# Kernel tuning notes

Hardware: AMD Instinct MI355X
Metric: run time of the kernel (lower is better)

## Reference

```python
import jax, jax.numpy as jnp
import numpy as np

# ---- cfg constants (JDE / YOLOv4-tracking style) ----
STRIDES = (8.0, 16.0, 32.0)
TRAIN_SIZE = 608.0
LEVELS = 3
NUM_ANCHORS = 4
EMB_DIM = 208
CONF_THRESH = 0.5
NMS_IOU = 0.45
K_LEVEL = 300   # proposals kept per level after confidence filtering
MAX_PROP = 500  # final padded proposal count per image
_ANCHORS = np.array([
    [[8, 24], [11, 34], [16, 48], [23, 68]],
    [[32, 96], [45, 135], [64, 192], [90, 271]],
    [[128, 384], [180, 540], [256, 640], [512, 640]],
], dtype=np.float32)  # [LEVELS, NUM_ANCHORS, 2] in pixels


def _decode_level(pred, emb, anchors_px, stride):
    """pred [B,A,H,W,6], emb [B,H,W,E] -> [B, A*H*W, 4+1+E] (xyxy in [0,1], conf, l2-norm emb)."""
    B, A, H, W, _ = pred.shape
    conf = jax.nn.softmax(pred[..., 4:6], axis=-1)[..., 1:2]  # [B,A,H,W,1]
    anc = anchors_px / stride  # anchors in grid units, [A,2]
    gy, gx = jnp.meshgrid(jnp.arange(H, dtype=pred.dtype),
                          jnp.arange(W, dtype=pred.dtype), indexing="ij")
    aw = anc[:, 0][:, None, None]  # [A,1,1]
    ah = anc[:, 1][:, None, None]
    # JDE-style delta decode: offsets scaled by anchor size, exp size decode
    x = pred[..., 0] * aw + gx
    y = pred[..., 1] * ah + gy
    w = jnp.exp(pred[..., 2]) * aw
    h = jnp.exp(pred[..., 3]) * ah
    scale = stride / TRAIN_SIZE  # back to pixels, then normalize by train size
    x1 = jnp.clip((x - 0.5 * w) * scale, 0.0, 1.0)
    y1 = jnp.clip((y - 0.5 * h) * scale, 0.0, 1.0)
    x2 = jnp.clip((x + 0.5 * w) * scale, 0.0, 1.0)
    y2 = jnp.clip((y + 0.5 * h) * scale, 0.0, 1.0)
    box = jnp.stack([x1, y1, x2, y2], axis=-1)  # [B,A,H,W,4]
    # tile embedding over anchors and l2-normalize (tf.math.l2_normalize, eps on sum of squares)
    pe = jnp.broadcast_to(emb[:, None], (B, A, H, W, emb.shape[-1]))
    n2 = jnp.sum(pe * pe, axis=-1, keepdims=True)
    pe = pe * jax.lax.rsqrt(jnp.maximum(n2, 1e-12))
    preds = jnp.concatenate([box, conf, pe], axis=-1)  # [B,A,H,W,4+1+E]
    return preds.reshape(B, A * H * W, preds.shape[-1])


def _conf_topk(props):
    """Confidence threshold + keep top K_LEVEL per image (zero-padded). props [B,N,D]."""
    s = props[..., 4]
    sm = jnp.where(s > CONF_THRESH, s, 0.0)
    top_s, top_i = jax.lax.top_k(sm, K_LEVEL)
    g = jnp.take_along_axis(props, top_i[..., None], axis=1)  # [B,K,D]
    return g * (top_s > 0.0)[..., None].astype(props.dtype)


def _nms_one(props):
    """Greedy NMS for one image. props [N,D] -> [MAX_PROP,D] zero-padded."""
    sc_in = props[:, 4]
    order = jnp.argsort(-sc_in)
    p = props[order]                      # sorted by score desc
    b, sc = p[:, :4], p[:, 4]
    N = b.shape[0]
    area = (b[:, 2] - b[:, 0]) * (b[:, 3] - b[:, 1])
    ix1 = jnp.maximum(b[:, None, 0], b[None, :, 0])
    iy1 = jnp.maximum(b[:, None, 1], b[None, :, 1])
    ix2 = jnp.minimum(b[:, None, 2], b[None, :, 2])
    iy2 = jnp.minimum(b[:, None, 3], b[None, :, 3])
    inter = jnp.clip(ix2 - ix1, 0.0) * jnp.clip(iy2 - iy1, 0.0)
    iou = inter / (area[:, None] + area[None, :] - inter + 1e-9)  # [N,N]
    idxs = jnp.arange(N)
    keep0 = sc > 0.0
    def step(keep, i):
        row = jnp.take(iou, i, axis=0)
        ki = jnp.take(keep, i)
        sup = ki & (row > NMS_IOU) & (idxs > i)
        return keep & jnp.logical_not(sup), None
    keep, _ = jax.lax.scan(step, keep0, idxs)
    keep = keep & (sc > 0.0)
    rank = jnp.cumsum(keep) - 1
    dest = jnp.where(keep & (rank < MAX_PROP), rank, MAX_PROP)  # out-of-range -> dropped
    out = jnp.zeros((MAX_PROP, p.shape[1]), p.dtype).at[dest].set(p, mode="drop")
    return out


def _forward(pred0, pred1, pred2, emb0, emb1, emb2):
    preds = (pred0, pred1, pred2)
    embs = (emb0, emb1, emb2)
    levels = []
    for i in range(LEVELS):
        pr = _decode_level(preds[i], embs[i], jnp.asarray(_ANCHORS[i]), STRIDES[i])
        levels.append(_conf_topk(pr))
    props = jnp.concatenate(levels, axis=1)        # [B, 3*K_LEVEL, 4+1+E]
    out = jax.vmap(_nms_one)(props)                # [B, MAX_PROP, 4+1+E]
    # entry_stop_gradients: grads only through non-zero (valid) entries
    mask = (jnp.sum(out[..., :4], axis=-1) != 0.0).astype(out.dtype)[..., None]
    return out * mask + jax.lax.stop_gradient(out) * (1.0 - mask)


def setup_inputs() -> dict:
    key = jax.random.key(0)
    ks = jax.random.split(key, 6)
    B = 16
    sizes = [76, 38, 19]  # TRAIN_SIZE // stride
    d = {}
    for i, hw in enumerate(sizes):
        d[f"pred{i}"] = jax.random.normal(ks[i], (B, NUM_ANCHORS, hw, hw, 6), jnp.float32)
        d[f"emb{i}"] = jax.random.normal(ks[3 + i], (B, hw, hw, EMB_DIM), jnp.float32)
    return d


def reference(pred0, pred1, pred2, emb0, emb1, emb2):
    return _forward(pred0, pred1, pred2, emb0, emb1, emb2)
```

## Files before the change

### kernel.cpp

```cpp
#include <hip/hip_runtime.h>

typedef unsigned long long u64;
typedef unsigned int u32;

#define KLVL 300
#define NPROP 900
#define MAXPROP 500
#define DDIM 213
#define EDIM 208

__constant__ float c_anc[3][4][2] = {
  {{1.0f, 3.0f}, {1.375f, 4.25f}, {2.0f, 6.0f}, {2.875f, 8.5f}},
  {{2.0f, 6.0f}, {2.8125f, 8.4375f}, {4.0f, 12.0f}, {5.625f, 16.9375f}},
  {{4.0f, 12.0f}, {5.625f, 16.875f}, {8.0f, 20.0f}, {16.0f, 20.0f}},
};
__constant__ float c_scale[3] = { (float)(8.0 / 608.0), (float)(16.0 / 608.0), (float)(32.0 / 608.0) };

__device__ __forceinline__ int level_H(int lvl) { return (lvl == 0) ? 76 : ((lvl == 1) ? 38 : 19); }

#define WS_SELS 0
#define WS_SELI (64*1024)
#define WS_CNT  (128*1024)
#define WS_BOX  (136*1024)
#define BOX_STRIDE 928
#define BOX_IMG (7*928)
#define WS_MASK (576*1024)
#define MASK_IMG (904*15)
#define WS_SRC  (2432*1024)

#define TK_T 1024
__global__ __launch_bounds__(TK_T) void topk_kernel(
    const float* __restrict__ pred0, const float* __restrict__ pred1, const float* __restrict__ pred2,
    float* __restrict__ sel_score, int* __restrict__ sel_idx, int* __restrict__ cnt)
{
  __shared__ float s_sc[23104];
  __shared__ u32 s_hist[4096];
  __shared__ u32 s_wt[16];
  __shared__ u64 s_wt64[16];
  __shared__ u32 s_sel[4];
  __shared__ float s_selS[KLVL];
  __shared__ int   s_selI[KLVL];

  const int lvl = blockIdx.x % 3;
  const int b = blockIdx.x / 3;
  const int t = threadIdx.x;
  const int lane = t & 63, wid = t >> 6;
  const int H = level_H(lvl);
  const int HW = H * H;
  const int N = 4 * HW;
  const float* pred = (lvl == 0) ? pred0 : ((lvl == 1) ? pred1 : pred2);
  const float* pb = pred + (size_t)b * N * 6;

  if (t == 0) s_sel[2] = 0;
  u32 nploc = 0;
  for (int n = t; n < N; n += TK_T) {
    float2 l = *reinterpret_cast<const float2*>(pb + (size_t)n * 6 + 4);
    float m = fmaxf(l.x, l.y);
    float e0 = expf(l.x - m), e1 = expf(l.y - m);
    float s = e1 / (e0 + e1);
    float sm = (s > 0.5f) ? s : 0.0f;
    s_sc[n] = sm;
    nploc += (sm > 0.0f) ? 1u : 0u;
  }
  __syncthreads();
  if (nploc) atomicAdd(&s_sel[2], nploc);
  __syncthreads();
  const u32 Npos = s_sel[2];
  const bool take_all = (Npos <= (u32)KLVL);
  u32 K = KLVL;
  u32 prefHi = 0, Tkey = 0;

  if (!take_all) {
    for (int pass = 0; pass < 2; ++pass) {
      for (int i = t; i < 4096; i += TK_T) s_hist[i] = 0;
      __syncthreads();
      for (int n = t; n < N; n += TK_T) {
        float v = s_sc[n];
        if (v <= 0.0f) continue;
        u32 key = __float_as_uint(v) - 0x3F000000u;
        if (pass == 0) atomicAdd(&s_hist[key >> 12], 1u);
        else if ((key >> 12) == prefHi) atomicAdd(&s_hist[key & 0xFFFu], 1u);
      }
      __syncthreads();
      const int btop = 4095 - 4 * t;
      u32 h0 = s_hist[btop], h1 = s_hist[btop - 1], h2 = s_hist[btop - 2], h3 = s_hist[btop - 3];
      u32 partial = h0 + h1 + h2 + h3;
      u32 incl = partial;
      #pragma unroll
      for (int off = 1; off < 64; off <<= 1) { u32 v2 = __shfl_up(incl, (unsigned)off, 64); if (lane >= off) incl += v2; }
      if (lane == 63) s_wt[wid] = incl;
      __syncthreads();
      u32 above = 0;
      for (int w2 = 0; w2 < wid; ++w2) above += s_wt[w2];
      u32 running = above + incl - partial;
      u32 hh0 = h0, hh1 = h1, hh2 = h2, hh3 = h3;
      if (hh0 && running < K && K <= running + hh0) { s_sel[0] = (u32)(btop);     s_sel[1] = K - running; }
      running += hh0;
      if (hh1 && running < K && K <= running + hh1) { s_sel[0] = (u32)(btop - 1); s_sel[1] = K - running; }
      running += hh1;
      if (hh2 && running < K && K <= running + hh2) { s_sel[0] = (u32)(btop - 2); s_sel[1] = K - running; }
      running += hh2;
      if (hh3 && running < K && K <= running + hh3) { s_sel[0] = (u32)(btop - 3); s_sel[1] = K - running; }
      __syncthreads();
      if (pass == 0) prefHi = s_sel[0];
      else Tkey = (prefHi << 12) | s_sel[0];
      K = s_sel[1];
      __syncthreads();
    }
  }
  const u32 need_ties = take_all ? 0u : K;
  const u32 G = take_all ? Npos : ((u32)KLVL - need_ties);
  const u32 Tbits = Tkey + 0x3F000000u;

  const int chunk = (N + TK_T - 1) / TK_T;
  const int lo = t * chunk;
  const int hi = (lo + chunk < N) ? (lo + chunk) : N;
  u32 cg = 0, ct = 0;
  for (int n = lo; n < hi; ++n) {
    float v = s_sc[n];
    if (v <= 0.0f) continue;
    u32 bits = __float_as_uint(v);
    if (take_all || bits > Tbits) cg++;
    else if (bits == Tbits) ct++;
  }
  u64 pc = ((u64)cg << 32) | (u64)ct;
  u64 incl64 = pc;
  #pragma unroll
  for (int off = 1; off < 64; off <<= 1) { u64 v2 = __shfl_up(incl64, (unsigned)off, 64); if (lane >= off) incl64 += v2; }
  if (lane == 63) s_wt64[wid] = incl64;
  __syncthreads();
  u64 ab = 0;
  for (int w2 = 0; w2 < wid; ++w2) ab += s_wt64[w2];
  u64 excl = ab + incl64 - pc;
  u32 g_pos = (u32)(excl >> 32);
  u32 t_pos = (u32)excl;
  for (int n = lo; n < hi; ++n) {
    float v = s_sc[n];
    if (v <= 0.0f) continue;
    u32 bits = __float_as_uint(v);
    if (take_all || bits > Tbits) {
      s_selS[g_pos] = v; s_selI[g_pos] = n; g_pos++;
    } else if (bits == Tbits) {
      if (t_pos < need_ties) { s_selS[G + t_pos] = v; s_selI[G + t_pos] = n; }
      t_pos++;
    }
  }
  __syncthreads();

  const u32 total = take_all ? Npos : (u32)KLVL;
  float* out_s = sel_score + (size_t)b * NPROP + (size_t)lvl * KLVL;
  int* out_i = sel_idx + (size_t)b * NPROP + (size_t)lvl * KLVL;
  if ((u32)t < total) {
    float sv = s_selS[t]; int iv = s_selI[t];
    u32 r = 0;
    for (u32 j = 0; j < total; ++j) {
      float sj = s_selS[j]; int ij = s_selI[j];
      r += ((sj > sv) || (sj == sv && ij < iv)) ? 1u : 0u;
    }
    out_s[r] = sv; out_i[r] = iv;
  }
  if (t == 0) cnt[b * 3 + lvl] = (int)total;
}

__global__ __launch_bounds__(1024) void rank_kernel(
    const float* __restrict__ pred0, const float* __restrict__ pred1, const float* __restrict__ pred2,
    const float* __restrict__ sel_score, const int* __restrict__ sel_idx, const int* __restrict__ cnt,
    float* __restrict__ ws_box)
{
  __shared__ float s_sc[NPROP];
  __shared__ int s_ix[NPROP];
  __shared__ int s_c[3];
  const int b = blockIdx.x, t = threadIdx.x;
  if (t < 3) s_c[t] = cnt[b * 3 + t];
  if (t < NPROP) { s_sc[t] = sel_score[(size_t)b * NPROP + t]; s_ix[t] = sel_idx[(size_t)b * NPROP + t]; }
  __syncthreads();
  if (t < NPROP) {
    int lvl = t / KLVL, pos = t - lvl * KLVL;
    if (pos < s_c[lvl]) {
      float sv = s_sc[t];
      u32 rank = (u32)pos;
      for (int ol = 0; ol < 3; ++ol) {
        if (ol == lvl) continue;
        int base = ol * KLVL, co = s_c[ol];
        int lo2 = 0, hi2 = co;
        if (ol < lvl) {
          while (lo2 < hi2) { int mid = (lo2 + hi2) >> 1; if (s_sc[base + mid] >= sv) lo2 = mid + 1; else hi2 = mid; }
        } else {
          while (lo2 < hi2) { int mid = (lo2 + hi2) >> 1; if (s_sc[base + mid] > sv) lo2 = mid + 1; else hi2 = mid; }
        }
        rank += (u32)lo2;
      }
      int n = s_ix[t];
      int Hl = level_H(lvl), HWl = Hl * Hl;
      int a = n / HWl, rem = n - a * HWl, gy = rem / Hl, gx = rem - gy * Hl;
      const float* pred = (lvl == 0) ? pred0 : ((lvl == 1) ? pred1 : pred2);
      const float* p = pred + ((size_t)b * 4 * HWl + (size_t)n) * 6;
      float p0 = p[0], p1 = p[1], p2 = p[2], p3 = p[3];
      float aw = c_anc[lvl][a][0], ah = c_anc[lvl][a][1];
      float x = p0 * aw + (float)gx;
      float y = p1 * ah + (float)gy;
      float wv = expf(p2) * aw;
      float hv = expf(p3) * ah;
      float sc = c_scale[lvl];
      float x1 = fminf(fmaxf((x - 0.5f * wv) * sc, 0.0f), 1.0f);
      float y1 = fminf(fmaxf((y - 0.5f * hv) * sc, 0.0f), 1.0f);
      float x2 = fminf(fmaxf((x + 0.5f * wv) * sc, 0.0f), 1.0f);
      float y2 = fminf(fmaxf((y + 0.5f * hv) * sc, 0.0f), 1.0f);
      float* Bx = ws_box + (size_t)b * BOX_IMG;
      Bx[rank] = x1;
      Bx[BOX_STRIDE + rank] = y1;
      Bx[2 * BOX_STRIDE + rank] = x2;
      Bx[3 * BOX_STRIDE + rank] = y2;
      Bx[4 * BOX_STRIDE + rank] = (x2 - x1) * (y2 - y1);
      Bx[5 * BOX_STRIDE + rank] = sv;
      ((int*)(Bx + 6 * BOX_STRIDE))[rank] = t;
    }
  }
}

__global__ __launch_bounds__(256) void mask_kernel(
    const float* __restrict__ ws_box, const int* __restrict__ cnt, u64* __restrict__ ws_mask)
{
  const int w = blockIdx.x, b = blockIdx.y, t = threadIdx.x;
  const float* B = ws_box + (size_t)b * BOX_IMG;
  const float* X1 = B, * Y1 = B + BOX_STRIDE, * X2 = B + 2 * BOX_STRIDE,
             * Y2 = B + 3 * BOX_STRIDE, * AR = B + 4 * BOX_STRIDE;
  const int Np = cnt[b * 3] + cnt[b * 3 + 1] + cnt[b * 3 + 2];
  __shared__ float jx1[64], jy1[64], jx2[64], jy2[64], jar[64];
  if (t < 64) {
    int j = w * 64 + t;
    if (j < Np) { jx1[t] = X1[j]; jy1[t] = Y1[j]; jx2[t] = X2[j]; jy2[t] = Y2[j]; jar[t] = AR[j]; }
  }
  __syncthreads();
  u64* mk = ws_mask + (size_t)b * MASK_IMG;
  const int jlim = min(64, Np - w * 64);
  for (int i = t; i < Np; i += 256) {
    u64 bits = 0;
    if (i < w * 64 + 63 && jlim > 0) {
      float xi1 = X1[i], yi1 = Y1[i], xi2 = X2[i], yi2 = Y2[i], ai = AR[i];
      for (int jj = 0; jj < jlim; ++jj) {
        int j = w * 64 + jj;
        if (j > i) {
          float xx1 = fmaxf(xi1, jx1[jj]);
          float yy1 = fmaxf(yi1, jy1[jj]);
          float xx2 = fminf(xi2, jx2[jj]);
          float yy2 = fminf(yi2, jy2[jj]);
          float iw = fmaxf(xx2 - xx1, 0.0f);
          float ih = fmaxf(yy2 - yy1, 0.0f);
          float inter = iw * ih;
          float iou = inter / (ai + jar[jj] - inter + 1e-9f);
          if (iou > 0.45f) bits |= (1ull << jj);
        }
      }
    }
    mk[(size_t)i * 15 + w] = bits;
  }
}

__global__ __launch_bounds__(256) void scan_kernel(
    const u64* __restrict__ ws_mask, const int* __restrict__ cnt, int* __restrict__ ws_src)
{
  __shared__ u64 sm[904 * 15];
  __shared__ u64 s_keep[15];
  __shared__ u32 s_pre[16];
  const int b = blockIdx.x, t = threadIdx.x;
  const int Np = cnt[b * 3] + cnt[b * 3 + 1] + cnt[b * 3 + 2];
  const u64* mk = ws_mask + (size_t)b * MASK_IMG;
  for (int i = t; i < Np * 15; i += 256) sm[i] = mk[i];
  __syncthreads();

  if (t < 64) {
    const int lane = t;
    const int lw = (lane < 15) ? lane : 0;
    u64 remv = 0;
    u64 r0 = sm[0 * 15 + lw], r1 = sm[1 * 15 + lw], r2 = sm[2 * 15 + lw], r3 = sm[3 * 15 + lw];
    const int Np4 = Np & ~3;
#define NMS_STEP(ii, rr) { \
      u32 bit_ = (u32)(remv >> ((ii) & 63)) & 1u; \
      u32 sup_ = (u32)__builtin_amdgcn_readlane((int)bit_, (ii) >> 6); \
      if (!sup_) remv |= (rr); }
    for (int i = 0; i < Np4; i += 4) {
      u64 n0 = sm[(size_t)(i + 4) * 15 + lw];
      u64 n1 = sm[(size_t)(i + 5) * 15 + lw];
      u64 n2 = sm[(size_t)(i + 6) * 15 + lw];
      u64 n3 = sm[(size_t)(i + 7) * 15 + lw];
      NMS_STEP(i, r0);
      NMS_STEP(i + 1, r1);
      NMS_STEP(i + 2, r2);
      NMS_STEP(i + 3, r3);
      r0 = n0; r1 = n1; r2 = n2; r3 = n3;
    }
    if (Np4 + 0 < Np) NMS_STEP(Np4 + 0, r0);
    if (Np4 + 1 < Np) NMS_STEP(Np4 + 1, r1);
    if (Np4 + 2 < Np) NMS_STEP(Np4 + 2, r2);
    if (Np4 + 3 < Np) NMS_STEP(Np4 + 3, r3);
#undef NMS_STEP
    if (lane < 15) {
      int base = lane << 6;
      u64 valid = 0;
      if (Np > base) {
        int r = Np - base;
        valid = (r >= 64) ? ~0ull : ((1ull << r) - 1ull);
      }
      s_keep[lane] = (~remv) & valid;
    }
  }
  __syncthreads();
  if (t == 0) {
    u32 run = 0;
    for (int w2 = 0; w2 < 15; ++w2) { s_pre[w2] = run; run += (u32)__popcll(s_keep[w2]); }
  }
  int* src = ws_src + b * MAXPROP;
  for (int r = t; r < MAXPROP; r += 256) src[r] = -1;
  __syncthreads();
  for (int i = t; i < Np; i += 256) {
    u64 kw = s_keep[i >> 6];
    if ((kw >> (i & 63)) & 1ull) {
      u32 rank = s_pre[i >> 6] + (u32)__popcll(kw & ((1ull << (i & 63)) - 1ull));
      if (rank < MAXPROP) src[rank] = i;
    }
  }
}

__global__ __launch_bounds__(256) void out_kernel(
    const float* __restrict__ emb0, const float* __restrict__ emb1, const float* __restrict__ emb2,
    const float* __restrict__ ws_box, const int* __restrict__ ws_src, const int* __restrict__ sel_idx,
    float* __restrict__ out)
{
  const int blk = blockIdx.x;
  const int b = blk / 125;
  const int r = (blk % 125) * 4 + (threadIdx.x >> 6);
  const int lane = threadIdx.x & 63;
  float* orow = out + ((size_t)b * MAXPROP + r) * DDIM;
  const int i = ws_src[b * MAXPROP + r];
  if (i < 0) {
    for (int c = lane; c < DDIM; c += 64) orow[c] = 0.0f;
    return;
  }
  const float* B = ws_box + (size_t)b * BOX_IMG;
  float x1 = B[i], y1 = B[BOX_STRIDE + i], x2 = B[2 * BOX_STRIDE + i], y2 = B[3 * BOX_STRIDE + i];
  float score = B[5 * BOX_STRIDE + i];
  int slot = ((const int*)(B + 6 * BOX_STRIDE))[i];
  int n = sel_idx[(size_t)b * NPROP + slot];
  int lvl = slot / KLVL;
  int Hl = level_H(lvl), HWl = Hl * Hl;
  int a = n / HWl, rem = n - a * HWl, gy = rem / Hl, gx = rem - gy * Hl;
  (void)a;
  const float* emb = (lvl == 0) ? emb0 : ((lvl == 1) ? emb1 : emb2);
  const float* e = emb + ((size_t)(b * Hl + gy) * Hl + gx) * EDIM;
  float v0 = e[lane], v1 = e[lane + 64], v2 = e[lane + 128];
  float v3 = (lane < 16) ? e[lane + 192] : 0.0f;
  float ss = v0 * v0 + v1 * v1 + v2 * v2 + v3 * v3;
  for (int off = 32; off > 0; off >>= 1) ss += __shfl_xor(ss, off, 64);
  float rs = 1.0f / sqrtf(fmaxf(ss, 1e-12f));
  if (lane == 0) {
    orow[0] = x1; orow[1] = y1; orow[2] = x2; orow[3] = y2; orow[4] = score;
  }
  orow[5 + lane] = v0 * rs;
  orow[5 + 64 + lane] = v1 * rs;
  orow[5 + 128 + lane] = v2 * rs;
  if (lane < 16) orow[5 + 192 + lane] = v3 * rs;
}

extern "C" void kernel_launch(void* const* d_in, const int* in_sizes, int n_in,
                              void* d_out, int out_size, void* d_ws, size_t ws_size,
                              hipStream_t stream) {
  const float* pred[3] = {nullptr, nullptr, nullptr};
  const float* emb[3] = {nullptr, nullptr, nullptr};
  for (int i = 0; i < n_in; ++i) {
    const float* p = (const float*)d_in[i];
    switch (in_sizes[i]) {
      case 2217984:  pred[0] = p; break;
      case 554496:   pred[1] = p; break;
      case 138624:   pred[2] = p; break;
      case 19222528: emb[0] = p; break;
      case 4805632:  emb[1] = p; break;
      case 1201408:  emb[2] = p; break;
      default: break;
    }
  }
  char* ws = (char*)d_ws;
  float* sel_score = (float*)(ws + WS_SELS);
  int* sel_idx = (int*)(ws + WS_SELI);
  int* cnt = (int*)(ws + WS_CNT);
  float* ws_box = (float*)(ws + WS_BOX);
  u64* ws_mask = (u64*)(ws + WS_MASK);
  int* ws_src = (int*)(ws + WS_SRC);

  topk_kernel<<<dim3(48), dim3(TK_T), 0, stream>>>(pred[0], pred[1], pred[2], sel_score, sel_idx, cnt);
  rank_kernel<<<dim3(16), dim3(1024), 0, stream>>>(pred[0], pred[1], pred[2], sel_score, sel_idx, cnt, ws_box);
  mask_kernel<<<dim3(15, 16), dim3(256), 0, stream>>>(ws_box, cnt, ws_mask);
  scan_kernel<<<dim3(16), dim3(256), 0, stream>>>(ws_mask, cnt, ws_src);
  out_kernel<<<dim3(2000), dim3(256), 0, stream>>>(emb[0], emb[1], emb[2], ws_box, ws_src, sel_idx, (float*)d_out);
}
```

Before: 276.7 us.

## Split confidence softmax into a wide score kernel before per-level top-k select

```diff
diff --git a/kernel.cpp b/kernel.cpp
--- a/kernel.cpp
+++ b/kernel.cpp
@@ -18,19 +18,44 @@
 
 __device__ __forceinline__ int level_H(int lvl) { return (lvl == 0) ? 76 : ((lvl == 1) ? 38 : 19); }
 
-#define WS_SELS 0
-#define WS_SELI (64*1024)
-#define WS_CNT  (128*1024)
-#define WS_BOX  (136*1024)
+#define SB_STRIDE 30336
+#define WS_SCORES 0
+#define WS_MASK   0
+#define MASK_IMG (904*15)
+#define WS_SELS (1941504)
+#define WS_SELI (WS_SELS + 57600)
+#define WS_CNT  (WS_SELI + 57600)
+#define WS_BOX  (WS_CNT + 256)
 #define BOX_STRIDE 928
 #define BOX_IMG (7*928)
-#define WS_MASK (576*1024)
-#define MASK_IMG (904*15)
-#define WS_SRC  (2432*1024)
+#define WS_SRC  (WS_BOX + 415744)
+
+__global__ __launch_bounds__(256) void score_kernel(
+    const float* __restrict__ pred0, const float* __restrict__ pred1, const float* __restrict__ pred2,
+    float* __restrict__ ws_scores)
+{
+  const int blk = blockIdx.x;
+  const int b = blk / 120;
+  const int r = blk % 120;
+  int lvl, rb, N, off;
+  const float* pred;
+  if (r < 91)       { lvl = 0; rb = r;       N = 23104; off = 0;     pred = pred0; }
+  else if (r < 114) { lvl = 1; rb = r - 91;  N = 5776;  off = 23104; pred = pred1; }
+  else              { lvl = 2; rb = r - 114; N = 1444;  off = 28880; pred = pred2; }
+  (void)lvl;
+  const int n = rb * 256 + (int)threadIdx.x;
+  if (n >= N) return;
+  const float* pb = pred + (size_t)b * N * 6;
+  float2 l = *reinterpret_cast<const float2*>(pb + (size_t)n * 6 + 4);
+  float m = fmaxf(l.x, l.y);
+  float e0 = expf(l.x - m), e1 = expf(l.y - m);
+  float s = e1 / (e0 + e1);
+  ws_scores[(size_t)b * SB_STRIDE + off + n] = (s > 0.5f) ? s : 0.0f;
+}
 
 #define TK_T 1024
-__global__ __launch_bounds__(TK_T) void topk_kernel(
-    const float* __restrict__ pred0, const float* __restrict__ pred1, const float* __restrict__ pred2,
+__global__ __launch_bounds__(TK_T) void select_kernel(
+    const float* __restrict__ ws_scores,
     float* __restrict__ sel_score, int* __restrict__ sel_idx, int* __restrict__ cnt)
 {
   __shared__ float s_sc[23104];
@@ -46,19 +71,14 @@
   const int t = threadIdx.x;
   const int lane = t & 63, wid = t >> 6;
   const int H = level_H(lvl);
-  const int HW = H * H;
-  const int N = 4 * HW;
-  const float* pred = (lvl == 0) ? pred0 : ((lvl == 1) ? pred1 : pred2);
-  const float* pb = pred + (size_t)b * N * 6;
+  const int N = 4 * H * H;
+  const int off = (lvl == 0) ? 0 : ((lvl == 1) ? 23104 : 28880);
+  const float* gs = ws_scores + (size_t)b * SB_STRIDE + off;
 
   if (t == 0) s_sel[2] = 0;
   u32 nploc = 0;
   for (int n = t; n < N; n += TK_T) {
-    float2 l = *reinterpret_cast<const float2*>(pb + (size_t)n * 6 + 4);
-    float m = fmaxf(l.x, l.y);
-    float e0 = expf(l.x - m), e1 = expf(l.y - m);
-    float s = e1 / (e0 + e1);
-    float sm = (s > 0.5f) ? s : 0.0f;
+    float sm = gs[n];
     s_sc[n] = sm;
     nploc += (sm > 0.0f) ? 1u : 0u;
   }
@@ -87,20 +107,19 @@
       u32 partial = h0 + h1 + h2 + h3;
       u32 incl = partial;
       #pragma unroll
-      for (int off = 1; off < 64; off <<= 1) { u32 v2 = __shfl_up(incl, (unsigned)off, 64); if (lane >= off) incl += v2; }
+      for (int off2 = 1; off2 < 64; off2 <<= 1) { u32 v2 = __shfl_up(incl, (unsigned)off2, 64); if (lane >= off2) incl += v2; }
       if (lane == 63) s_wt[wid] = incl;
       __syncthreads();
       u32 above = 0;
       for (int w2 = 0; w2 < wid; ++w2) above += s_wt[w2];
       u32 running = above + incl - partial;
-      u32 hh0 = h0, hh1 = h1, hh2 = h2, hh3 = h3;
-      if (hh0 && running < K && K <= running + hh0) { s_sel[0] = (u32)(btop);     s_sel[1] = K - running; }
-      running += hh0;
-      if (hh1 && running < K && K <= running + hh1) { s_sel[0] = (u32)(btop - 1); s_sel[1] = K - running; }
-      running += hh1;
-      if (hh2 && running < K && K <= running + hh2) { s_sel[0] = (u32)(btop - 2); s_sel[1] = K - running; }
-      running += hh2;
-      if (hh3 && running < K && K <= running + hh3) { s_sel[0] = (u32)(btop - 3); s_sel[1] = K - running; }
+      if (h0 && running < K && K <= running + h0) { s_sel[0] = (u32)(btop);     s_sel[1] = K - running; }
+      running += h0;
+      if (h1 && running < K && K <= running + h1) { s_sel[0] = (u32)(btop - 1); s_sel[1] = K - running; }
+      running += h1;
+      if (h2 && running < K && K <= running + h2) { s_sel[0] = (u32)(btop - 2); s_sel[1] = K - running; }
+      running += h2;
+      if (h3 && running < K && K <= running + h3) { s_sel[0] = (u32)(btop - 3); s_sel[1] = K - running; }
       __syncthreads();
       if (pass == 0) prefHi = s_sel[0];
       else Tkey = (prefHi << 12) | s_sel[0];
@@ -126,7 +145,7 @@
   u64 pc = ((u64)cg << 32) | (u64)ct;
   u64 incl64 = pc;
   #pragma unroll
-  for (int off = 1; off < 64; off <<= 1) { u64 v2 = __shfl_up(incl64, (unsigned)off, 64); if (lane >= off) incl64 += v2; }
+  for (int off2 = 1; off2 < 64; off2 <<= 1) { u64 v2 = __shfl_up(incl64, (unsigned)off2, 64); if (lane >= off2) incl64 += v2; }
   if (lane == 63) s_wt64[wid] = incl64;
   __syncthreads();
   u64 ab = 0;
@@ -159,6 +178,7 @@
     }
     out_s[r] = sv; out_i[r] = iv;
   }
+  for (u32 s2 = total + (u32)t; s2 < (u32)KLVL; s2 += TK_T) { out_s[s2] = 0.0f; out_i[s2] = 0; }
   if (t == 0) cnt[b * 3 + lvl] = (int)total;
 }
 
@@ -380,14 +400,16 @@
     }
   }
   char* ws = (char*)d_ws;
+  float* ws_scores = (float*)(ws + WS_SCORES);
+  u64* ws_mask = (u64*)(ws + WS_MASK);
   float* sel_score = (float*)(ws + WS_SELS);
   int* sel_idx = (int*)(ws + WS_SELI);
   int* cnt = (int*)(ws + WS_CNT);
   float* ws_box = (float*)(ws + WS_BOX);
-  u64* ws_mask = (u64*)(ws + WS_MASK);
   int* ws_src = (int*)(ws + WS_SRC);
 
-  topk_kernel<<<dim3(48), dim3(TK_T), 0, stream>>>(pred[0], pred[1], pred[2], sel_score, sel_idx, cnt);
+  score_kernel<<<dim3(1920), dim3(256), 0, stream>>>(pred[0], pred[1], pred[2], ws_scores);
+  select_kernel<<<dim3(48), dim3(TK_T), 0, stream>>>(ws_scores, sel_score, sel_idx, cnt);
   rank_kernel<<<dim3(16), dim3(1024), 0, stream>>>(pred[0], pred[1], pred[2], sel_score, sel_idx, cnt, ws_box);
   mask_kernel<<<dim3(15, 16), dim3(256), 0, stream>>>(ws_box, cnt, ws_mask);
   scan_kernel<<<dim3(16), dim3(256), 0, stream>>>(ws_mask, cnt, ws_src);
```

New measurement: 270.3 us. 1.02x faster.
